# Kernel optimization log

Hardware: AMD Instinct MI355X
Metric: run time of the kernel (lower is better)

Reference implementation:

```python
import jax, jax.numpy as jnp
import numpy as np

TAN30 = float(np.tan(np.pi / 6.0))
KNN_K = 3
KNN_CHUNK = 2000  # divides 32000 and 96000


def onera_transform(pos):
    new_x = pos[:, 0] - TAN30 * pos[:, 1]
    pos = jnp.concatenate([new_x[:, None], pos[:, 1:]], axis=1)
    return pos * (1.0 + (1.0 / 0.56 - 1.0) * (pos[:, 1:2] / 1.1963))


def knn(pos_x, pos_y, k=KNN_K, chunk=KNN_CHUNK):
    # For each query in pos_y, find k nearest points in pos_x (squared distance).
    x2 = jnp.sum(pos_x * pos_x, axis=-1)  # [Nx]

    def body(q):  # q: [chunk, d]
        d = jnp.sum(q * q, axis=-1, keepdims=True) - 2.0 * q @ pos_x.T + x2[None, :]
        neg_d, idx = jax.lax.top_k(-d, k)
        return -neg_d, idx

    qs = pos_y.reshape(-1, chunk, pos_y.shape[1])
    d, idx = jax.lax.map(body, qs)
    return d.reshape(-1, k), idx.reshape(-1, k)


def knn_interpolate(x, pos_x, pos_y, k=KNN_K):
    # PyG knn_interpolate: inverse-squared-distance weights, computed under no_grad.
    d2, idx = knn(jax.lax.stop_gradient(pos_x), jax.lax.stop_gradient(pos_y), k)
    w = 1.0 / jnp.maximum(d2, 1e-16)  # [Ny, k]
    num = jnp.einsum('nk,nkc->nc', w, x[idx])
    return num / jnp.sum(w, axis=-1, keepdims=True)


def onera_interp(x, pos_x, pos_y):
    return knn_interpolate(x, onera_transform(pos_x), onera_transform(pos_y))


def gcn_conv(x, edge_index, W, b):
    n = x.shape[0]
    xw = x @ W
    loop = jnp.arange(n, dtype=edge_index.dtype)
    row = jnp.concatenate([edge_index[0], loop])  # source
    col = jnp.concatenate([edge_index[1], loop])  # target
    deg = jax.ops.segment_sum(jnp.ones(row.shape[0], dtype=xw.dtype), col, num_segments=n)
    dinv = jax.lax.rsqrt(deg)  # deg >= 1 due to self loops
    norm = dinv[row] * dinv[col]
    out = jax.ops.segment_sum(xw[row] * norm[:, None], col, num_segments=n)
    return out + b


def setup_inputs() -> dict:
    key = jax.random.key(0)
    ks = jax.random.split(key, 24)
    N0, N1, N2 = 16000, 32000, 96000
    E0, E1, E2 = 128000, 256000, 768000
    LC, HC, D, OC = 64, 128, 3, 5
    IC = HC + D  # 131

    def w(k, shape):
        return (jax.random.normal(k, shape, dtype=jnp.float32) / np.sqrt(shape[0])).astype(jnp.float32)

    inp = {
        'latent': jax.random.normal(ks[0], (N0, LC), dtype=jnp.float32),
        'pos_0': jax.random.uniform(ks[1], (N0, D), dtype=jnp.float32),
        'pos_1': jax.random.uniform(ks[2], (N1, D), dtype=jnp.float32),
        'pos_2': jax.random.uniform(ks[3], (N2, D), dtype=jnp.float32),
        'W_lin': w(ks[4], (LC, HC)), 'b_lin': jnp.zeros((HC,), jnp.float32),
        'W0': w(ks[5], (IC, HC)), 'b0': jnp.zeros((HC,), jnp.float32),
        'W1': w(ks[6], (IC, HC)), 'b1': jnp.zeros((HC,), jnp.float32),
        'W2': w(ks[7], (IC, HC)), 'b2': jnp.zeros((HC,), jnp.float32),
        'W3': w(ks[8], (IC, HC)), 'b3': jnp.zeros((HC,), jnp.float32),
        'W4': w(ks[9], (IC, OC)), 'b4': jnp.zeros((OC,), jnp.float32),
        'edge_index_0': jax.random.randint(ks[10], (2, E0), 0, N0, dtype=jnp.int32),
        'edge_index_1': jax.random.randint(ks[11], (2, E1), 0, N1, dtype=jnp.int32),
        'edge_index_2': jax.random.randint(ks[12], (2, E2), 0, N2, dtype=jnp.int32),
    }
    return inp


def reference(latent, pos_0, pos_1, pos_2, W_lin, b_lin, W0, b0, W1, b1, W2, b2, W3, b3, W4, b4,
              edge_index_0, edge_index_1, edge_index_2):
    selu = jax.nn.selu
    x = selu(latent @ W_lin + b_lin)
    # two convs at coarsest level
    x = selu(gcn_conv(jnp.concatenate([x, pos_0], axis=1), edge_index_0, W0, b0))
    x = selu(gcn_conv(jnp.concatenate([x, pos_0], axis=1), edge_index_0, W1, b1))
    # pool 0: level 0 -> 1
    x = onera_interp(x, pos_0, pos_1)
    x = selu(gcn_conv(jnp.concatenate([x, pos_1], axis=1), edge_index_1, W2, b2))
    # pool 1: level 1 -> 2
    x = onera_interp(x, pos_1, pos_2)
    x = selu(gcn_conv(jnp.concatenate([x, pos_2], axis=1), edge_index_2, W3, b3))
    # output conv (no activation)
    out = gcn_conv(jnp.concatenate([x, pos_2], axis=1), edge_index_2, W4, b4)
    return out
```

## Files before the change

kernel.cpp:

```cpp
#include <hip/hip_runtime.h>
#include <math.h>

#define TAN30f 0.57735026918962576f
#define SELU_SCALE 1.0507009873554805f
#define SELU_ALPHA 1.6732632423543772f

#define MAXC 65536
#define MAXG 40
#define BBOXBLK 64
#define PPC_T 0.4f

__device__ __forceinline__ float selu_f(float x) {
    return SELU_SCALE * (x > 0.0f ? x : SELU_ALPHA * expm1f(x));
}

struct GP {
    float ox, oy, oz, ihx, ihy, ihz, hmin2, pad;
    int Gx, Gy, Gz, maxG;
};

template<int FIC, bool HAS_POS, bool BIAS_SELU, bool ROWSCALE>
__global__ __launch_bounds__(256) void k_matmul128(
    const float* __restrict__ X, const float* __restrict__ P,
    const float* __restrict__ W, const float* __restrict__ bias,
    const float* __restrict__ rs,
    float* __restrict__ Y, int N)
{
    constexpr int ICT = FIC + (HAS_POS ? 3 : 0);
    __shared__ float xs[16][ICT + 1];
    int row0 = blockIdx.x * 16;

    for (int idx = threadIdx.x; idx < 16 * FIC; idx += 256) {
        int r = idx / FIC, c = idx % FIC;
        int gr = row0 + r;
        xs[r][c] = (gr < N) ? X[gr * FIC + c] : 0.0f;
    }
    if (HAS_POS) {
        for (int idx = threadIdx.x; idx < 16 * 3; idx += 256) {
            int r = idx / 3, c = idx % 3;
            int gr = row0 + r;
            xs[r][FIC + c] = (gr < N) ? P[gr * 3 + c] : 0.0f;
        }
    }
    __syncthreads();

    int col = threadIdx.x & 127;
    int half = threadIdx.x >> 7;
    float acc[8];
#pragma unroll
    for (int r = 0; r < 8; ++r) acc[r] = 0.0f;

#pragma unroll 4
    for (int i = 0; i < ICT; ++i) {
        float wv = W[i * 128 + col];
#pragma unroll
        for (int r = 0; r < 8; ++r)
            acc[r] = fmaf(xs[half * 8 + r][i], wv, acc[r]);
    }

    float bv = BIAS_SELU ? bias[col] : 0.0f;
#pragma unroll
    for (int r = 0; r < 8; ++r) {
        int gr = row0 + half * 8 + r;
        if (gr < N) {
            float v = acc[r];
            if (BIAS_SELU) v = selu_f(v + bv);
            if (ROWSCALE) v *= rs[gr];
            Y[gr * 128 + col] = v;
        }
    }
}

__global__ void k_hist3(const int* __restrict__ c0, int E0, int* __restrict__ n0,
                        const int* __restrict__ c1, int E1, int* __restrict__ n1,
                        const int* __restrict__ c2, int E2, int* __restrict__ n2) {
    int i = blockIdx.x * 256 + threadIdx.x;
    if (i < E0) atomicAdd(&n0[c0[i]], 1);
    else if (i < E0 + E1) atomicAdd(&n1[c1[i - E0]], 1);
    else if (i < E0 + E1 + E2) atomicAdd(&n2[c2[i - E0 - E1]], 1);
}

__global__ __launch_bounds__(256) void k_scan1t(
    const int* __restrict__ in0, int* __restrict__ out0, float* __restrict__ dva, int n0a,
    const int* __restrict__ in1, int* __restrict__ out1, float* __restrict__ dvb, int n1a,
    const int* __restrict__ in2, int* __restrict__ out2, float* __restrict__ dvc, int n2a,
    int* __restrict__ bsum, int nbmax)
{
    int y = blockIdx.y;
    const int* in = y == 0 ? in0 : (y == 1 ? in1 : in2);
    int* out = y == 0 ? out0 : (y == 1 ? out1 : out2);
    float* dv = y == 0 ? dva : (y == 1 ? dvb : dvc);
    int n = y == 0 ? n0a : (y == 1 ? n1a : n2a);
    __shared__ int s[256];
    int tid = threadIdx.x;
    int base = blockIdx.x * 1024 + tid * 4;
    int a[4];
#pragma unroll
    for (int k = 0; k < 4; ++k) a[k] = (base + k < n) ? in[base + k] : 0;
#pragma unroll
    for (int k = 0; k < 4; ++k)
        if (base + k < n) dv[base + k] = rsqrtf((float)a[k] + 1.0f);
    int t = a[0] + a[1] + a[2] + a[3];
    s[tid] = t;
    __syncthreads();
    for (int off = 1; off < 256; off <<= 1) {
        int x = (tid >= off) ? s[tid - off] : 0;
        __syncthreads();
        s[tid] += x;
        __syncthreads();
    }
    int run = s[tid] - t;
#pragma unroll
    for (int k = 0; k < 4; ++k) {
        if (base + k < n) out[base + k] = run;
        run += a[k];
    }
    if (tid == 255) bsum[y * nbmax + blockIdx.x] = s[255];
}

__global__ void k_scan2(int* __restrict__ bsum, int nb) {
    if (threadIdx.x == 0) {
        int* b = bsum + blockIdx.x * nb;
        int run = 0;
        for (int i = 0; i < nb; ++i) { int v = b[i]; b[i] = run; run += v; }
    }
}

__global__ void k_scan3t(int* __restrict__ rp0, int* __restrict__ cu0, int E0, int n0a,
                         int* __restrict__ rp1, int* __restrict__ cu1, int E1, int n1a,
                         int* __restrict__ rp2, int* __restrict__ cu2, int E2, int n2a,
                         const int* __restrict__ bsum, int nbmax) {
    int y = blockIdx.y;
    int* rp = y == 0 ? rp0 : (y == 1 ? rp1 : rp2);
    int* cu = y == 0 ? cu0 : (y == 1 ? cu1 : cu2);
    int E = y == 0 ? E0 : (y == 1 ? E1 : E2);
    int n = y == 0 ? n0a : (y == 1 ? n1a : n2a);
    const int* bs = bsum + y * nbmax;
    int i = blockIdx.x * 256 + threadIdx.x;
    if (i < n) {
        int v = rp[i] + bs[i >> 10];
        rp[i] = v;
        cu[i] = v;
    }
    if (i == 0) rp[n] = E;
}

__global__ void k_scatter3(const int* __restrict__ ei0, int E0, int* __restrict__ cu0, int* __restrict__ cs0,
                           const int* __restrict__ ei1, int E1, int* __restrict__ cu1, int* __restrict__ cs1,
                           const int* __restrict__ ei2, int E2, int* __restrict__ cu2, int* __restrict__ cs2) {
    int i = blockIdx.x * 256 + threadIdx.x;
    const int* ei; int E; int* cur; int* csr; int e;
    if (i < E0)               { ei = ei0; E = E0; cur = cu0; csr = cs0; e = i; }
    else if (i < E0 + E1)     { ei = ei1; E = E1; cur = cu1; csr = cs1; e = i - E0; }
    else if (i < E0 + E1 + E2){ ei = ei2; E = E2; cur = cu2; csr = cs2; e = i - E0 - E1; }
    else return;
    int r = ei[e], c = ei[E + e];
    int p = atomicAdd(&cur[c], 1);
    csr[p] = r;
}

__global__ __launch_bounds__(256) void k_gather128(
    const int* __restrict__ rowptr, const int* __restrict__ csr,
    const float4* __restrict__ xws4, const float* __restrict__ dv,
    const float4* __restrict__ bias4, float4* __restrict__ out4, int N)
{
    int t = blockIdx.x * 256 + threadIdx.x;
    int node = t >> 5, c4 = t & 31;
    if (node >= N) return;
    int s = rowptr[node], e = rowptr[node + 1];
    float4 acc = xws4[(size_t)node * 32 + c4];
    for (int i = s; i < e; ++i) {
        int src = csr[i];
        float4 v = xws4[(size_t)src * 32 + c4];
        acc.x += v.x; acc.y += v.y; acc.z += v.z; acc.w += v.w;
    }
    float d = dv[node];
    float4 b = bias4[c4];
    float4 o;
    o.x = selu_f(fmaf(acc.x, d, b.x));
    o.y = selu_f(fmaf(acc.y, d, b.y));
    o.z = selu_f(fmaf(acc.z, d, b.z));
    o.w = selu_f(fmaf(acc.w, d, b.w));
    out4[(size_t)node * 32 + c4] = o;
}

__global__ __launch_bounds__(256) void k_gather5(
    const int* __restrict__ rowptr, const int* __restrict__ csr,
    const float* __restrict__ xws, const float* __restrict__ dv,
    const float* __restrict__ bias, float* __restrict__ out, int N)
{
    int t = blockIdx.x * 256 + threadIdx.x;
    int node = t >> 3, ch = t & 7;
    if (node >= N || ch >= 5) return;
    int s = rowptr[node], e = rowptr[node + 1];
    float acc = xws[(size_t)node * 5 + ch];
    for (int i = s; i < e; ++i) {
        int src = csr[i];
        acc += xws[(size_t)src * 5 + ch];
    }
    out[(size_t)node * 5 + ch] = acc * dv[node] + bias[ch];
}

__global__ void k_transform3(const float* __restrict__ p0, float4* __restrict__ t0, int n0,
                             const float* __restrict__ p1, float4* __restrict__ t1, int n1,
                             const float* __restrict__ p2, float4* __restrict__ t2, int n2) {
    int i = blockIdx.x * 256 + threadIdx.x;
    const float* pos; float4* tp; int li;
    if (i < n0) { pos = p0; tp = t0; li = i; }
    else if (i < n0 + n1) { pos = p1; tp = t1; li = i - n0; }
    else if (i < n0 + n1 + n2) { pos = p2; tp = t2; li = i - n0 - n1; }
    else return;
    float x = pos[li * 3 + 0], y = pos[li * 3 + 1], z = pos[li * 3 + 2];
    float nx = x - TAN30f * y;
    float f = 1.0f + (1.0f / 0.56f - 1.0f) * (y / 1.1963f);
    float X = nx * f, Y = y * f, Z = z * f;
    tp[li] = make_float4(X, Y, Z, (X * X + Y * Y) + Z * Z);
}

__global__ __launch_bounds__(256) void k_bbox2(const float4* __restrict__ tpa, int na,
                                               const float4* __restrict__ tpb, int nb,
                                               float* __restrict__ bbp) {
    const float4* tp = blockIdx.y ? tpb : tpa;
    int n = blockIdx.y ? nb : na;
    __shared__ float red[6][256];
    float mn0 = 3.4e38f, mn1 = 3.4e38f, mn2 = 3.4e38f;
    float mx0 = -3.4e38f, mx1 = -3.4e38f, mx2 = -3.4e38f;
    for (int i = blockIdx.x * 256 + threadIdx.x; i < n; i += gridDim.x * 256) {
        float4 t = tp[i];
        mn0 = fminf(mn0, t.x); mx0 = fmaxf(mx0, t.x);
        mn1 = fminf(mn1, t.y); mx1 = fmaxf(mx1, t.y);
        mn2 = fminf(mn2, t.z); mx2 = fmaxf(mx2, t.z);
    }
    int tid = threadIdx.x;
    red[0][tid] = mn0; red[1][tid] = mn1; red[2][tid] = mn2;
    red[3][tid] = mx0; red[4][tid] = mx1; red[5][tid] = mx2;
    __syncthreads();
    for (int off = 128; off > 0; off >>= 1) {
        if (tid < off) {
#pragma unroll
            for (int k = 0; k < 3; ++k) {
                red[k][tid] = fminf(red[k][tid], red[k][tid + off]);
                red[3 + k][tid] = fmaxf(red[3 + k][tid], red[3 + k][tid + off]);
            }
        }
        __syncthreads();
    }
    if (tid == 0) {
        float* o = bbp + (blockIdx.y * BBOXBLK + blockIdx.x) * 6;
#pragma unroll
        for (int k = 0; k < 3; ++k) {
            o[k] = red[k][0];
            o[3 + k] = red[3 + k][0];
        }
    }
}

__global__ void k_gridparams2(const float* __restrict__ bbp, int na, int nb,
                              GP* __restrict__ gps) {
    if (threadIdx.x != 0) return;
    int set = blockIdx.x;
    const float* bp = bbp + set * BBOXBLK * 6;
    int n = set ? nb : na;
    GP* gp = gps + set;
    float mn[3] = {3.4e38f, 3.4e38f, 3.4e38f};
    float mx[3] = {-3.4e38f, -3.4e38f, -3.4e38f};
    for (int i = 0; i < BBOXBLK; ++i) {
#pragma unroll
        for (int k = 0; k < 3; ++k) {
            mn[k] = fminf(mn[k], bp[i * 6 + k]);
            mx[k] = fmaxf(mx[k], bp[i * 6 + 3 + k]);
        }
    }
    float e[3], o[3];
#pragma unroll
    for (int k = 0; k < 3; ++k) {
        float ext = fmaxf(mx[k] - mn[k], 1e-6f);
        float padv = ext * 1e-4f + 1e-6f;
        o[k] = mn[k] - padv;
        e[k] = ext + 2.0f * padv;
    }
    float T = (float)n * PPC_T;
    float s = cbrtf(T / (e[0] * e[1] * e[2]));
    int G[3];
#pragma unroll
    for (int k = 0; k < 3; ++k) {
        int g = (int)ceilf(e[k] * s);
        G[k] = g < 1 ? 1 : (g > MAXG ? MAXG : g);
    }
    float h[3];
#pragma unroll
    for (int k = 0; k < 3; ++k) h[k] = e[k] / (float)G[k];
    float hmin = fminf(h[0], fminf(h[1], h[2]));
    gp->ox = o[0]; gp->oy = o[1]; gp->oz = o[2];
    gp->ihx = (float)G[0] / e[0]; gp->ihy = (float)G[1] / e[1]; gp->ihz = (float)G[2] / e[2];
    gp->hmin2 = hmin * hmin;
    gp->Gx = G[0]; gp->Gy = G[1]; gp->Gz = G[2];
    gp->maxG = max(G[0], max(G[1], G[2]));
}

__device__ __forceinline__ int cell_of(float4 t, const GP* gp) {
    int cx = min(max((int)((t.x - gp->ox) * gp->ihx), 0), gp->Gx - 1);
    int cy = min(max((int)((t.y - gp->oy) * gp->ihy), 0), gp->Gy - 1);
    int cz = min(max((int)((t.z - gp->oz) * gp->ihz), 0), gp->Gz - 1);
    return (cz * gp->Gy + cy) * gp->Gx + cx;
}

__global__ void k_cellid4(const float4* __restrict__ tp0, int N0,
                          const float4* __restrict__ tp1, int N1,
                          const float4* __restrict__ tp2, int N2,
                          int* __restrict__ gcell0, int* __restrict__ qcell1,
                          int* __restrict__ gcell1, int* __restrict__ qcell2,
                          int* __restrict__ cnt, const GP* __restrict__ gps) {
    int i = blockIdx.x * 256 + threadIdx.x;
    const float4* tp; const GP* gp; int* cellout; int* cn; int li;
    if (i < N0)                { tp = tp0; gp = gps;     cellout = gcell0; cn = cnt;            li = i; }
    else if (i < N0 + N1)      { tp = tp1; gp = gps;     cellout = qcell1; cn = cnt + MAXC;     li = i - N0; }
    else if (i < N0 + 2 * N1)  { tp = tp1; gp = gps + 1; cellout = gcell1; cn = cnt + 2 * MAXC; li = i - N0 - N1; }
    else if (i < N0 + 2 * N1 + N2) { tp = tp2; gp = gps + 1; cellout = qcell2; cn = cnt + 3 * MAXC; li = i - N0 - 2 * N1; }
    else return;
    int cid = cell_of(tp[li], gp);
    cellout[li] = cid;
    atomicAdd(&cn[cid], 1);
}

__global__ __launch_bounds__(256) void k_scan1c(const int* __restrict__ cnt,
                                                int* __restrict__ row,
                                                int* __restrict__ bsum, int nb) {
    const int* in = cnt + blockIdx.y * MAXC;
    int* out = row + blockIdx.y * (MAXC + 1);
    __shared__ int s[256];
    int tid = threadIdx.x;
    int base = blockIdx.x * 1024 + tid * 4;
    int a[4];
#pragma unroll
    for (int k = 0; k < 4; ++k) a[k] = (base + k < MAXC) ? in[base + k] : 0;
    int t = a[0] + a[1] + a[2] + a[3];
    s[tid] = t;
    __syncthreads();
    for (int off = 1; off < 256; off <<= 1) {
        int x = (tid >= off) ? s[tid - off] : 0;
        __syncthreads();
        s[tid] += x;
        __syncthreads();
    }
    int run = s[tid] - t;
#pragma unroll
    for (int k = 0; k < 4; ++k) {
        if (base + k < MAXC) out[base + k] = run;
        run += a[k];
    }
    if (tid == 255) bsum[blockIdx.y * nb + blockIdx.x] = s[255];
}

__global__ void k_scan3c(int* __restrict__ row, int* __restrict__ cur,
                         const int* __restrict__ bsum, int nb, int4 E4) {
    int y = blockIdx.y;
    int* rp = row + y * (MAXC + 1);
    int* cu = cur + y * MAXC;
    const int* bs = bsum + y * nb;
    int E = (y == 0) ? E4.x : (y == 1) ? E4.y : (y == 2) ? E4.z : E4.w;
    int i = blockIdx.x * 256 + threadIdx.x;
    if (i < MAXC) {
        int v = rp[i] + bs[i >> 10];
        rp[i] = v;
        cu[i] = v;
    }
    if (i == 0) rp[MAXC] = E;
}

__global__ void k_scatter4(const float4* __restrict__ tp0, int N0,
                           const float4* __restrict__ tp1, int N1,
                           const float4* __restrict__ tp2, int N2,
                           const int* __restrict__ gcell0, const int* __restrict__ qcell1,
                           const int* __restrict__ gcell1, const int* __restrict__ qcell2,
                           int* __restrict__ cur,
                           float4* __restrict__ gpts0, float4* __restrict__ gpts1,
                           int* __restrict__ qorder1, int* __restrict__ qorder2) {
    int i = blockIdx.x * 256 + threadIdx.x;
    if (i < N0) {
        int p = atomicAdd(&cur[gcell0[i]], 1);
        float4 t = tp0[i];
        t.w = __int_as_float(i);
        gpts0[p] = t;
    } else if (i < N0 + N1) {
        int j = i - N0;
        int p = atomicAdd(&cur[MAXC + qcell1[j]], 1);
        qorder1[p] = j;
    } else if (i < N0 + 2 * N1) {
        int j = i - N0 - N1;
        int p = atomicAdd(&cur[2 * MAXC + gcell1[j]], 1);
        float4 t = tp1[j];
        t.w = __int_as_float(j);
        gpts1[p] = t;
    } else if (i < N0 + 2 * N1 + N2) {
        int j = i - N0 - 2 * N1;
        int p = atomicAdd(&cur[3 * MAXC + qcell2[j]], 1);
        qorder2[p] = j;
    }
}

__global__ __launch_bounds__(256) void k_knn_grid2(
    const float4* __restrict__ tpq1, int N1, const int* __restrict__ qorder1,
    const float4* __restrict__ gpts0, const int* __restrict__ crow0,
    int* __restrict__ oidx1, float* __restrict__ ow1,
    const float4* __restrict__ tpq2, int N2, const int* __restrict__ qorder2,
    const float4* __restrict__ gpts1, const int* __restrict__ crow1,
    int* __restrict__ oidx2, float* __restrict__ ow2,
    const GP* __restrict__ gps)
{
    int t = blockIdx.x * 256 + threadIdx.x;
    const float4* tpq; const int* qord; const float4* gpts; const int* crow;
    const GP* gp; int* oidx; float* ow; int slot; int Nq;
    if (t < N1) {
        tpq = tpq1; qord = qorder1; gpts = gpts0; crow = crow0;
        gp = gps; oidx = oidx1; ow = ow1; slot = t; Nq = N1;
    } else {
        tpq = tpq2; qord = qorder2; gpts = gpts1; crow = crow1;
        gp = gps + 1; oidx = oidx2; ow = ow2; slot = t - N1; Nq = N2;
    }
    bool active = slot < Nq;
    int qi = active ? qord[slot] : 0;

    float ox = gp->ox, oy = gp->oy, oz = gp->oz;
    float ihx = gp->ihx, ihy = gp->ihy, ihz = gp->ihz;
    float hmin2 = gp->hmin2;
    int Gx = gp->Gx, Gy = gp->Gy, Gz = gp->Gz, maxG = gp->maxG;

    float qx = 0, qy = 0, qz = 0, q2 = 0;
    if (active) { float4 tq = tpq[qi]; qx = tq.x; qy = tq.y; qz = tq.z; q2 = tq.w; }
    int cx = min(max((int)((qx - ox) * ihx), 0), Gx - 1);
    int cy = min(max((int)((qy - oy) * ihy), 0), Gy - 1);
    int cz = min(max((int)((qz - oz) * ihz), 0), Gz - 1);

    float d0 = 3.4e38f, d1 = 3.4e38f, d2 = 3.4e38f;
    int j0 = 0x7FFFFFFF, j1 = 0x7FFFFFFF, j2 = 0x7FFFFFFF;

    auto insert = [&](float d, int id) {
        if (d < d2 || (d == d2 && id < j2)) {
            if (d < d1 || (d == d1 && id < j1)) {
                d2 = d1; j2 = j1;
                if (d < d0 || (d == d0 && id < j0)) {
                    d1 = d0; j1 = j0; d0 = d; j0 = id;
                } else { d1 = d; j1 = id; }
            } else { d2 = d; j2 = id; }
        }
    };
    auto proc = [&](float4 p) {
        int id = __float_as_int(p.w);
        float px2 = fmaf(p.z, p.z, fmaf(p.y, p.y, p.x * p.x));
        float dot = fmaf(p.z, qz, fmaf(p.y, qy, p.x * qx));
        float d = (q2 - 2.0f * dot) + px2;
        insert(d, id);
    };
    auto scan_range = [&](int s, int e) {
        int i = s;
        for (; i + 3 < e; i += 4) {
            float4 pa = gpts[i], pb = gpts[i + 1], pc = gpts[i + 2], pd = gpts[i + 3];
            proc(pa); proc(pb); proc(pc); proc(pd);
        }
        for (; i < e; ++i) { float4 p = gpts[i]; proc(p); }
    };
    auto scan_cells = [&](int zz, int yy, int xlo, int xhi) {
        int base = (zz * Gy + yy) * Gx;
        scan_range(crow[base + xlo], crow[base + xhi + 1]);
    };

    {
        int xlo = max(cx - 1, 0), xhi = min(cx + 1, Gx - 1);
        int rs[9], re[9];
#pragma unroll
        for (int k = 0; k < 9; ++k) {
            int zz = cz + k / 3 - 1, yy = cy + k % 3 - 1;
            bool ok = active && zz >= 0 && zz < Gz && yy >= 0 && yy < Gy;
            int base = ok ? (zz * Gy + yy) * Gx : 0;
            int a = crow[base + (ok ? xlo : 0)];
            int b = crow[base + (ok ? xhi + 1 : 0)];
            rs[k] = ok ? a : 0;
            re[k] = ok ? b : 0;
        }
#pragma unroll
        for (int k = 0; k < 9; ++k) scan_range(rs[k], re[k]);
    }
    bool done = !active || (d2 < hmin2);

    for (int r = 2; r <= maxG; ++r) {
        if (__all(done)) break;
        if (!done) {
            int xlo = max(cx - r, 0), xhi = min(cx + r, Gx - 1);
            for (int zz = max(cz - r, 0); zz <= min(cz + r, Gz - 1); ++zz)
                for (int yy = max(cy - r, 0); yy <= min(cy + r, Gy - 1); ++yy) {
                    if (max(abs(zz - cz), abs(yy - cy)) == r) {
                        scan_cells(zz, yy, xlo, xhi);
                    } else {
                        if (cx - r >= 0)      scan_cells(zz, yy, cx - r, cx - r);
                        if (cx + r <= Gx - 1) scan_cells(zz, yy, cx + r, cx + r);
                    }
                }
            done = d2 < hmin2 * (float)(r * r);
        }
    }

    if (active) {
        float w0 = 1.0f / fmaxf(d0, 1e-16f);
        float w1 = 1.0f / fmaxf(d1, 1e-16f);
        float w2 = 1.0f / fmaxf(d2, 1e-16f);
        float s = w0 + w1 + w2;
        oidx[qi * 3 + 0] = j0; oidx[qi * 3 + 1] = j1; oidx[qi * 3 + 2] = j2;
        ow[qi * 4 + 0] = w0; ow[qi * 4 + 1] = w1; ow[qi * 4 + 2] = w2; ow[qi * 4 + 3] = s;
    }
}

__global__ void k_interp(const float4* __restrict__ x4, const int* __restrict__ idx,
                         const float* __restrict__ w, float4* __restrict__ y4, int Nq) {
    int t = blockIdx.x * 256 + threadIdx.x;
    if (t >= Nq * 32) return;
    int j = t >> 5, c = t & 31;
    int i0 = idx[j * 3], i1 = idx[j * 3 + 1], i2 = idx[j * 3 + 2];
    float w0 = w[j * 4], w1 = w[j * 4 + 1], w2 = w[j * 4 + 2], s = w[j * 4 + 3];
    float inv = 1.0f / s;
    float4 a = x4[(size_t)i0 * 32 + c];
    float4 b = x4[(size_t)i1 * 32 + c];
    float4 d = x4[(size_t)i2 * 32 + c];
    float4 o;
    o.x = (w0 * a.x + w1 * b.x + w2 * d.x) * inv;
    o.y = (w0 * a.y + w1 * b.y + w2 * d.y) * inv;
    o.z = (w0 * a.z + w1 * b.z + w2 * d.z) * inv;
    o.w = (w0 * a.w + w1 * b.w + w2 * d.w) * inv;
    y4[(size_t)j * 32 + c] = o;
}

__global__ __launch_bounds__(256) void k_matmul5(const float* __restrict__ X, const float* __restrict__ P,
                                                 const float* __restrict__ W, const float* __restrict__ rs,
                                                 float* __restrict__ Y, int N) {
    __shared__ float xs[32][132];
    __shared__ float ws[131 * 5];
    int row0 = blockIdx.x * 32;
    for (int idx = threadIdx.x; idx < 131 * 5; idx += 256) ws[idx] = W[idx];
    for (int idx = threadIdx.x; idx < 32 * 128; idx += 256) {
        int r = idx >> 7, c = idx & 127;
        xs[r][c] = X[(size_t)(row0 + r) * 128 + c];
    }
    for (int idx = threadIdx.x; idx < 32 * 3; idx += 256) {
        int r = idx / 3, c = idx % 3;
        xs[r][128 + c] = P[(row0 + r) * 3 + c];
    }
    __syncthreads();
    int r = threadIdx.x >> 3;
    int c = threadIdx.x & 7;
    if (c < 5) {
        float acc = 0.0f;
        for (int i = 0; i < 131; ++i) acc = fmaf(xs[r][i], ws[i * 5 + c], acc);
        Y[(size_t)(row0 + r) * 5 + c] = acc * rs[row0 + r];
    }
}

extern "C" void kernel_launch(void* const* d_in, const int* in_sizes, int n_in,
                              void* d_out, int out_size, void* d_ws, size_t ws_size,
                              hipStream_t stream) {
    const float* latent = (const float*)d_in[0];
    const float* pos0   = (const float*)d_in[1];
    const float* pos1   = (const float*)d_in[2];
    const float* pos2   = (const float*)d_in[3];
    const float* W_lin  = (const float*)d_in[4];
    const float* b_lin  = (const float*)d_in[5];
    const float* W0 = (const float*)d_in[6];  const float* b0 = (const float*)d_in[7];
    const float* W1 = (const float*)d_in[8];  const float* b1 = (const float*)d_in[9];
    const float* W2 = (const float*)d_in[10]; const float* b2 = (const float*)d_in[11];
    const float* W3 = (const float*)d_in[12]; const float* b3 = (const float*)d_in[13];
    const float* W4 = (const float*)d_in[14]; const float* b4 = (const float*)d_in[15];
    const int* ei0 = (const int*)d_in[16];
    const int* ei1 = (const int*)d_in[17];
    const int* ei2 = (const int*)d_in[18];
    float* out = (float*)d_out;

    const int N0 = in_sizes[1] / 3, N1 = in_sizes[2] / 3, N2 = in_sizes[3] / 3;
    const int E0 = in_sizes[16] / 2, E1 = in_sizes[17] / 2, E2 = in_sizes[18] / 2;

    char* wsp = (char*)d_ws;
    auto alloc = [&](size_t bytes) {
        char* p = wsp;
        wsp += (bytes + 255) & ~size_t(255);
        return p;
    };
    float*    A       = (float*)alloc((size_t)N2 * 128 * 4);
    float*    Bb      = (float*)alloc((size_t)N2 * 128 * 4);
    float4*   tp0     = (float4*)alloc((size_t)N0 * 16);
    float4*   tp1     = (float4*)alloc((size_t)N1 * 16);
    float4*   tp2     = (float4*)alloc((size_t)N2 * 16);
    float*    dv0     = (float*)alloc((size_t)N0 * 4);
    float*    dv1     = (float*)alloc((size_t)N1 * 4);
    float*    dv2     = (float*)alloc((size_t)N2 * 4);
    int*      cnt012  = (int*)  alloc((size_t)(N0 + N1 + N2) * 4);
    int*      cnt0 = cnt012, *cnt1 = cnt012 + N0, *cnt2 = cnt012 + N0 + N1;
    int*      rp0     = (int*)  alloc(((size_t)N0 + 1) * 4);
    int*      rp1     = (int*)  alloc(((size_t)N1 + 1) * 4);
    int*      rp2     = (int*)  alloc(((size_t)N2 + 1) * 4);
    int*      cur0    = (int*)  alloc((size_t)N0 * 4);
    int*      cur1    = (int*)  alloc((size_t)N1 * 4);
    int*      cur2    = (int*)  alloc((size_t)N2 * 4);
    int*      csr0    = (int*)  alloc((size_t)E0 * 4);
    int*      csr1    = (int*)  alloc((size_t)E1 * 4);
    int*      csr2    = (int*)  alloc((size_t)E2 * 4);
    int*      bsum    = (int*)  alloc(4096);
    float*    xw5     = (float*)alloc((size_t)N2 * 5 * 4);
    float*    bbp     = (float*)alloc((size_t)2 * BBOXBLK * 6 * 4);
    GP*       gps     = (GP*)   alloc(2 * sizeof(GP));
    int*      knncnt  = (int*)  alloc((size_t)4 * MAXC * 4);
    int*      knnrow  = (int*)  alloc((size_t)4 * (MAXC + 1) * 4);
    int*      knncur  = (int*)  alloc((size_t)4 * MAXC * 4);
    int*      gcell0  = (int*)  alloc((size_t)N0 * 4);
    int*      gcell1  = (int*)  alloc((size_t)N1 * 4);
    int*      qcell1  = (int*)  alloc((size_t)N1 * 4);
    int*      qcell2  = (int*)  alloc((size_t)N2 * 4);
    float4*   gpts0   = (float4*)alloc((size_t)N0 * 16);
    float4*   gpts1   = (float4*)alloc((size_t)N1 * 16);
    int*      qorder1 = (int*)  alloc((size_t)N1 * 4);
    int*      qorder2 = (int*)  alloc((size_t)N2 * 4);
    int*      kidx1   = (int*)  alloc((size_t)N1 * 3 * 4);
    float*    kw1     = (float*)alloc((size_t)N1 * 4 * 4);
    int*      kidx2   = (int*)  alloc((size_t)N2 * 3 * 4);
    float*    kw2     = (float*)alloc((size_t)N2 * 4 * 4);

    auto cdiv = [](int a, int b) { return (a + b - 1) / b; };

    k_transform3<<<cdiv(N0 + N1 + N2, 256), 256, 0, stream>>>(pos0, tp0, N0, pos1, tp1, N1,
                                                              pos2, tp2, N2);

    {
        k_bbox2<<<dim3(BBOXBLK, 2), 256, 0, stream>>>(tp0, N0, tp1, N1, bbp);
        k_gridparams2<<<2, 64, 0, stream>>>(bbp, N0, N1, gps);
        hipMemsetAsync(knncnt, 0, (size_t)4 * MAXC * 4, stream);
        int tot = N0 + 2 * N1 + N2;
        k_cellid4<<<cdiv(tot, 256), 256, 0, stream>>>(tp0, N0, tp1, N1, tp2, N2,
                                                      gcell0, qcell1, gcell1, qcell2,
                                                      knncnt, gps);
        int nbc = cdiv(MAXC, 1024);
        k_scan1c<<<dim3(nbc, 4), 256, 0, stream>>>(knncnt, knnrow, bsum, nbc);
        k_scan2<<<4, 64, 0, stream>>>(bsum, nbc);
        k_scan3c<<<dim3(cdiv(MAXC, 256), 4), 256, 0, stream>>>(knnrow, knncur, bsum, nbc,
                                                               make_int4(N0, N1, N1, N2));
        k_scatter4<<<cdiv(tot, 256), 256, 0, stream>>>(tp0, N0, tp1, N1, tp2, N2,
                                                       gcell0, qcell1, gcell1, qcell2,
                                                       knncur, gpts0, gpts1, qorder1, qorder2);
        k_knn_grid2<<<cdiv(N1 + N2, 256), 256, 0, stream>>>(
            tp1, N1, qorder1, gpts0, knnrow, kidx1, kw1,
            tp2, N2, qorder2, gpts1, knnrow + 2 * (MAXC + 1), kidx2, kw2, gps);
    }

    {
        hipMemsetAsync(cnt012, 0, (size_t)(N0 + N1 + N2) * 4, stream);
        k_hist3<<<cdiv(E0 + E1 + E2, 256), 256, 0, stream>>>(ei0 + E0, E0, cnt0,
                                                             ei1 + E1, E1, cnt1,
                                                             ei2 + E2, E2, cnt2);
        int nbmax = cdiv(N2, 1024);
        k_scan1t<<<dim3(nbmax, 3), 256, 0, stream>>>(cnt0, rp0, dv0, N0,
                                                     cnt1, rp1, dv1, N1,
                                                     cnt2, rp2, dv2, N2, bsum, nbmax);
        k_scan2<<<3, 64, 0, stream>>>(bsum, nbmax);
        k_scan3t<<<dim3(cdiv(N2, 256), 3), 256, 0, stream>>>(rp0, cur0, E0, N0,
                                                             rp1, cur1, E1, N1,
                                                             rp2, cur2, E2, N2, bsum, nbmax);
        k_scatter3<<<cdiv(E0 + E1 + E2, 256), 256, 0, stream>>>(ei0, E0, cur0, csr0,
                                                                ei1, E1, cur1, csr1,
                                                                ei2, E2, cur2, csr2);
    }

    auto conv128 = [&](const float* x, const float* pos, int N,
                       const int* rp, const int* csr, const float* dv,
                       const float* W, const float* b, float* xws, float* outb) {
        k_matmul128<128, true, false, true><<<cdiv(N, 16), 256, 0, stream>>>(x, pos, W, nullptr, dv, xws, N);
        k_gather128<<<cdiv(N * 32, 256), 256, 0, stream>>>(rp, csr, (const float4*)xws, dv,
                                                           (const float4*)b, (float4*)outb, N);
    };

    k_matmul128<64, false, true, false><<<cdiv(N0, 16), 256, 0, stream>>>(latent, nullptr, W_lin, b_lin, nullptr, A, N0);

    conv128(A, pos0, N0, rp0, csr0, dv0, W0, b0, Bb, A);
    conv128(A, pos0, N0, rp0, csr0, dv0, W1, b1, Bb, A);

    k_interp<<<cdiv(N1 * 32, 256), 256, 0, stream>>>((const float4*)A, kidx1, kw1, (float4*)Bb, N1);

    conv128(Bb, pos1, N1, rp1, csr1, dv1, W2, b2, A, Bb);

    k_interp<<<cdiv(N2 * 32, 256), 256, 0, stream>>>((const float4*)Bb, kidx2, kw2, (float4*)A, N2);

    conv128(A, pos2, N2, rp2, csr2, dv2, W3, b3, Bb, A);

    k_matmul5<<<cdiv(N2, 32), 256, 0, stream>>>(A, pos2, W4, dv2, xw5, N2);
    k_gather5<<<cdiv(N2 * 8, 256), 256, 0, stream>>>(rp2, csr2, xw5, dv2, b4, out, N2);
}
```

Measured before the change: 873.1 us.

## Fuse kNN interpolation into matmul input load and raise grid cell occupancy threshold

Removes the separate k_interp kernel by computing the inverse-distance-weighted 3-neighbor interpolation directly while loading rows into shared memory in k_matmul128. This drops the write and re-read of the interpolated N1x128 and N2x128 intermediate buffers. The fused loads are scalar per-element gathers rather than float4, and the weights and indices are reloaded for every channel. The grid points-per-cell threshold PPC_T is also doubled, which changes the kNN spatial grid resolution.

```diff
diff --git a/kernel.cpp b/kernel.cpp
--- a/kernel.cpp
+++ b/kernel.cpp
@@ -8,7 +8,7 @@
 #define MAXC 65536
 #define MAXG 40
 #define BBOXBLK 64
-#define PPC_T 0.4f
+#define PPC_T 0.8f
 
 __device__ __forceinline__ float selu_f(float x) {
     return SELU_SCALE * (x > 0.0f ? x : SELU_ALPHA * expm1f(x));
@@ -19,11 +19,12 @@
     int Gx, Gy, Gz, maxG;
 };
 
-template<int FIC, bool HAS_POS, bool BIAS_SELU, bool ROWSCALE>
+template<int FIC, bool HAS_POS, bool BIAS_SELU, bool ROWSCALE, bool INTERP>
 __global__ __launch_bounds__(256) void k_matmul128(
     const float* __restrict__ X, const float* __restrict__ P,
     const float* __restrict__ W, const float* __restrict__ bias,
     const float* __restrict__ rs,
+    const int* __restrict__ kidx, const float* __restrict__ kw,
     float* __restrict__ Y, int N)
 {
     constexpr int ICT = FIC + (HAS_POS ? 3 : 0);
@@ -33,7 +34,20 @@
     for (int idx = threadIdx.x; idx < 16 * FIC; idx += 256) {
         int r = idx / FIC, c = idx % FIC;
         int gr = row0 + r;
-        xs[r][c] = (gr < N) ? X[gr * FIC + c] : 0.0f;
+        float v = 0.0f;
+        if (gr < N) {
+            if (INTERP) {
+                int i0 = kidx[gr * 3], i1 = kidx[gr * 3 + 1], i2 = kidx[gr * 3 + 2];
+                float w0 = kw[gr * 4], w1 = kw[gr * 4 + 1], w2 = kw[gr * 4 + 2];
+                float inv = 1.0f / kw[gr * 4 + 3];
+                float num = w0 * X[(size_t)i0 * FIC + c] + w1 * X[(size_t)i1 * FIC + c]
+                          + w2 * X[(size_t)i2 * FIC + c];
+                v = num * inv;
+            } else {
+                v = X[(size_t)gr * FIC + c];
+            }
+        }
+        xs[r][c] = v;
     }
     if (HAS_POS) {
         for (int idx = threadIdx.x; idx < 16 * 3; idx += 256) {
@@ -66,7 +80,7 @@
             float v = acc[r];
             if (BIAS_SELU) v = selu_f(v + bv);
             if (ROWSCALE) v *= rs[gr];
-            Y[gr * 128 + col] = v;
+            Y[(size_t)gr * 128 + col] = v;
         }
     }
 }
@@ -508,25 +522,6 @@
         oidx[qi * 3 + 0] = j0; oidx[qi * 3 + 1] = j1; oidx[qi * 3 + 2] = j2;
         ow[qi * 4 + 0] = w0; ow[qi * 4 + 1] = w1; ow[qi * 4 + 2] = w2; ow[qi * 4 + 3] = s;
     }
-}
-
-__global__ void k_interp(const float4* __restrict__ x4, const int* __restrict__ idx,
-                         const float* __restrict__ w, float4* __restrict__ y4, int Nq) {
-    int t = blockIdx.x * 256 + threadIdx.x;
-    if (t >= Nq * 32) return;
-    int j = t >> 5, c = t & 31;
-    int i0 = idx[j * 3], i1 = idx[j * 3 + 1], i2 = idx[j * 3 + 2];
-    float w0 = w[j * 4], w1 = w[j * 4 + 1], w2 = w[j * 4 + 2], s = w[j * 4 + 3];
-    float inv = 1.0f / s;
-    float4 a = x4[(size_t)i0 * 32 + c];
-    float4 b = x4[(size_t)i1 * 32 + c];
-    float4 d = x4[(size_t)i2 * 32 + c];
-    float4 o;
-    o.x = (w0 * a.x + w1 * b.x + w2 * d.x) * inv;
-    o.y = (w0 * a.y + w1 * b.y + w2 * d.y) * inv;
-    o.z = (w0 * a.z + w1 * b.z + w2 * d.z) * inv;
-    o.w = (w0 * a.w + w1 * b.w + w2 * d.w) * inv;
-    y4[(size_t)j * 32 + c] = o;
 }
 
 __global__ __launch_bounds__(256) void k_matmul5(const float* __restrict__ X, const float* __restrict__ P,
@@ -665,26 +660,27 @@
                                                                 ei2, E2, cur2, csr2);
     }
 
-    auto conv128 = [&](const float* x, const float* pos, int N,
-                       const int* rp, const int* csr, const float* dv,
-                       const float* W, const float* b, float* xws, float* outb) {
-        k_matmul128<128, true, false, true><<<cdiv(N, 16), 256, 0, stream>>>(x, pos, W, nullptr, dv, xws, N);
-        k_gather128<<<cdiv(N * 32, 256), 256, 0, stream>>>(rp, csr, (const float4*)xws, dv,
-                                                           (const float4*)b, (float4*)outb, N);
-    };
-
-    k_matmul128<64, false, true, false><<<cdiv(N0, 16), 256, 0, stream>>>(latent, nullptr, W_lin, b_lin, nullptr, A, N0);
-
-    conv128(A, pos0, N0, rp0, csr0, dv0, W0, b0, Bb, A);
-    conv128(A, pos0, N0, rp0, csr0, dv0, W1, b1, Bb, A);
-
-    k_interp<<<cdiv(N1 * 32, 256), 256, 0, stream>>>((const float4*)A, kidx1, kw1, (float4*)Bb, N1);
-
-    conv128(Bb, pos1, N1, rp1, csr1, dv1, W2, b2, A, Bb);
-
-    k_interp<<<cdiv(N2 * 32, 256), 256, 0, stream>>>((const float4*)Bb, kidx2, kw2, (float4*)A, N2);
-
-    conv128(A, pos2, N2, rp2, csr2, dv2, W3, b3, Bb, A);
+    k_matmul128<64, false, true, false, false><<<cdiv(N0, 16), 256, 0, stream>>>(
+        latent, nullptr, W_lin, b_lin, nullptr, nullptr, nullptr, A, N0);
+
+    k_matmul128<128, true, false, true, false><<<cdiv(N0, 16), 256, 0, stream>>>(
+        A, pos0, W0, nullptr, dv0, nullptr, nullptr, Bb, N0);
+    k_gather128<<<cdiv(N0 * 32, 256), 256, 0, stream>>>(rp0, csr0, (const float4*)Bb, dv0,
+                                                        (const float4*)b0, (float4*)A, N0);
+    k_matmul128<128, true, false, true, false><<<cdiv(N0, 16), 256, 0, stream>>>(
+        A, pos0, W1, nullptr, dv0, nullptr, nullptr, Bb, N0);
+    k_gather128<<<cdiv(N0 * 32, 256), 256, 0, stream>>>(rp0, csr0, (const float4*)Bb, dv0,
+                                                        (const float4*)b1, (float4*)A, N0);
+
+    k_matmul128<128, true, false, true, true><<<cdiv(N1, 16), 256, 0, stream>>>(
+        A, pos1, W2, nullptr, dv1, kidx1, kw1, Bb, N1);
+    k_gather128<<<cdiv(N1 * 32, 256), 256, 0, stream>>>(rp1, csr1, (const float4*)Bb, dv1,
+                                                        (const float4*)b2, (float4*)A, N1);
+
+    k_matmul128<128, true, false, true, true><<<cdiv(N2, 16), 256, 0, stream>>>(
+        A, pos2, W3, nullptr, dv2, kidx2, kw2, Bb, N2);
+    k_gather128<<<cdiv(N2 * 32, 256), 256, 0, stream>>>(rp2, csr2, (const float4*)Bb, dv2,
+                                                        (const float4*)b3, (float4*)A, N2);
 
     k_matmul5<<<cdiv(N2, 32), 256, 0, stream>>>(A, pos2, W4, dv2, xw5, N2);
     k_gather5<<<cdiv(N2 * 8, 256), 256, 0, stream>>>(rp2, csr2, xw5, dv2, b4, out, N2);
```

After: 831.5 us. 4.8% less time.
